# Kernel optimization log

Measured on AMD Instinct MI355X. Metric: run time of the kernel, lower is better.

## Reference

```python
import jax, jax.numpy as jnp
import numpy as np

LAMBDA_VIOLATION = 0.5
NUM_SAMPLES = 128
EPS = 1e-09
B = 4096
K_MAX = 128
NK_MAX = 128
# unique (n, k, m) parameter combos, cycled over the batch
COMBOS = np.array([[256, 128, 3], [192, 96, 3], [224, 112, 4], [160, 80, 2]], dtype=np.int64)


def setup_inputs() -> dict:
    key = jax.random.key(0)
    k1, k2, k3 = jax.random.split(key, 3)
    y_pred = jax.random.uniform(k1, (B, 1), minval=0.5, maxval=8.0, dtype=jnp.float32)
    y_true = jax.random.uniform(k2, (B, 1), minval=0.5, maxval=8.0, dtype=jnp.float32)
    P_padded = jax.random.normal(k3, (B, K_MAX, NK_MAX), dtype=jnp.float32)
    params = jnp.asarray(COMBOS[np.arange(B) % len(COMBOS)])  # [B, 3] int64
    return {"y_pred": y_pred, "y_true": y_true, "P_padded": P_padded, "params": params}


def reference(y_pred, y_true, P_padded, params):
    # LogMSE in base 2
    log2_pred = jnp.log2(jnp.clip(y_pred, EPS))
    log2_true = jnp.log2(jnp.clip(y_true, EPS))
    loss_logmse = jnp.mean((log2_true - log2_pred) ** 2)

    batch = P_padded.shape[0]
    p_np = np.asarray(params)  # int params are concrete constants
    combos, inverse = np.unique(p_np, axis=0, return_inverse=True)

    total_penalty = jnp.asarray(0.0, dtype=y_pred.dtype)
    xkey = jax.random.key(42)
    for i in range(combos.shape[0]):
        n, k, m = int(combos[i, 0]), int(combos[i, 1]), int(combos[i, 2])
        idx = np.nonzero(inverse == i)[0]
        if m + 1 > n or k <= 0 or n - k < 0 or idx.size == 0:
            continue
        g = idx.size
        P_actual = P_padded[idx, :k, : n - k]            # [g, k, n-k]
        X = jax.random.normal(jax.random.fold_in(xkey, i), (g, NUM_SAMPLES, k), dtype=y_pred.dtype)
        # G = [I_k | P_actual]  =>  C = X @ G = [X | X @ P_actual]
        C = jnp.concatenate([X, jnp.einsum('bsk,bkp->bsp', X, P_actual)], axis=2)  # [g, S, n]
        mags = jnp.abs(C)
        top, _ = jax.lax.top_k(mags, m + 1)              # [g, S, m+1] sorted descending
        hm = top[..., 0] / (top[..., m] + EPS)           # c_max / c_m
        max_hm = jnp.max(hm, axis=1)                     # [g]
        penalty = jax.nn.relu(max_hm - y_pred[idx].squeeze(-1))
        total_penalty = total_penalty + jnp.sum(penalty)

    loss_violation = total_penalty / batch
    total_loss = loss_logmse + LAMBDA_VIOLATION * loss_violation
    return total_loss, loss_logmse, loss_violation
```

## Files before the change

kernel.cpp:

```cpp
#include <hip/hip_runtime.h>
#include <stdint.h>

typedef short bf16x8 __attribute__((ext_vector_type(8)));
typedef float f32x4 __attribute__((ext_vector_type(4)));

__host__ __device__ inline uint32_t rotl32(uint32_t v, int d) {
  return (v << d) | (v >> (32 - d));
}

__host__ __device__ inline void tf2x32(uint32_t k0, uint32_t k1,
                                       uint32_t x0, uint32_t x1,
                                       uint32_t& o0, uint32_t& o1) {
  uint32_t ks0 = k0, ks1 = k1, ks2 = k0 ^ k1 ^ 0x1BD11BDAu;
  x0 += ks0; x1 += ks1;
#define TF_R(r) { x0 += x1; x1 = rotl32(x1, (r)); x1 ^= x0; }
  TF_R(13) TF_R(15) TF_R(26) TF_R(6)
  x0 += ks1; x1 += ks2 + 1u;
  TF_R(17) TF_R(29) TF_R(16) TF_R(24)
  x0 += ks2; x1 += ks0 + 2u;
  TF_R(13) TF_R(15) TF_R(26) TF_R(6)
  x0 += ks0; x1 += ks1 + 3u;
  TF_R(17) TF_R(29) TF_R(16) TF_R(24)
  x0 += ks1; x1 += ks2 + 4u;
  TF_R(13) TF_R(15) TF_R(26) TF_R(6)
  x0 += ks2; x1 += ks0 + 5u;
#undef TF_R
  o0 = x0; o1 = x1;
}

__device__ __forceinline__ float erfinv_xla(float x) {
  float w = -__logf(fmaf(-x, x, 1.0f));
  float p;
  if (w < 5.0f) {
    w = w - 2.5f;
    p = 2.81022636e-08f;
    p = fmaf(p, w, 3.43273939e-07f);
    p = fmaf(p, w, -3.5233877e-06f);
    p = fmaf(p, w, -4.39150654e-06f);
    p = fmaf(p, w, 0.00021858087f);
    p = fmaf(p, w, -0.00125372503f);
    p = fmaf(p, w, -0.00417768164f);
    p = fmaf(p, w, 0.246640727f);
    p = fmaf(p, w, 1.50140941f);
  } else {
    w = sqrtf(w) - 3.0f;
    p = -0.000200214257f;
    p = fmaf(p, w, 0.000100950558f);
    p = fmaf(p, w, 0.00134934322f);
    p = fmaf(p, w, -0.00367342844f);
    p = fmaf(p, w, 0.00573950773f);
    p = fmaf(p, w, -0.0076224613f);
    p = fmaf(p, w, 0.00943887047f);
    p = fmaf(p, w, 1.00167406f);
    p = fmaf(p, w, 2.83297682f);
  }
  return p * x;
}

__device__ __forceinline__ float bits_to_normal(uint32_t bits) {
  uint32_t fb = (bits >> 9) | 0x3F800000u;
  float f = __uint_as_float(fb) - 1.0f;
  const float lo = -0.99999994f;
  float u = fmaf(f, 1.0f - lo, lo);
  u = fmaxf(lo, u);
  return 1.41421356f * erfinv_xla(u);
}

__device__ __forceinline__ uint32_t cvt_pk_bf16(float lo, float hi) {
  uint32_t r;
  asm("v_cvt_pk_bf16_f32 %0, %1, %2" : "=v"(r) : "v"(lo), "v"(hi));
  return r;
}

__device__ __forceinline__ float bf2f_s(short h) {
  return __uint_as_float(((uint32_t)(uint16_t)h) << 16);
}

__device__ __forceinline__ bf16x8 pack8(const float (&r)[8]) {
  union { bf16x8 v; uint32_t u[4]; } o;
#pragma unroll
  for (int p = 0; p < 4; ++p)
    o.u[p] = cvt_pk_bf16(r[2 * p], r[2 * p + 1]);
  return o.v;
}

template <int T>
__device__ __forceinline__ void insT(float (&t)[T], float v) {
  if constexpr (T == 1) {
    t[0] = fmaxf(t[0], v);
  } else {
    float t0o = t[0], t1o = t[1];
    t[0] = fmaxf(t0o, v);
    t[1] = __builtin_amdgcn_fmed3f(v, t0o, t1o);
    float a = fminf(fminf(v, t0o), t1o);
#pragma unroll
    for (int q = 2; q < T; ++q) {
      float tq = t[q];
      t[q] = fmaxf(tq, a);
      a = fminf(tq, a);
    }
  }
}

template <int K, int KP, int T>
__device__ void process_combo(const float* __restrict__ Pp,
                              const float* __restrict__ yp,
                              const float* __restrict__ yt,
                              float* __restrict__ accum,
                              int ofs, uint32_t key0, uint32_t key1,
                              int rp, char* sm) {
  constexpr int KSTEPS = KP / 32;
  constexpr int NCH = (K + 31) / 32;
  constexpr int PH = K / 2;
  constexpr int ITERS = PH / 4;
  constexpr int XSTR = KP + 8;
  constexpr int XSTRU = XSTR / 2;
  constexpr int XROW_U = 64 * XSTRU;
  constexpr int REGION = 2 * 64 * XSTR * 2;
  constexpr bool SKIP1 = (K % 32) == 16;
  constexpr uint32_t HALF = 65536u * (uint32_t)K;

  const int tid = threadIdx.x;
  const int wave = tid >> 6;
  const int lane = tid & 63;
  const int quad = lane >> 4;
  const int l15 = lane & 15;
  const int row = wave >> 1;
  const int msub = (wave & 1) * 32;

  const int b0 = 4 * rp + ofs;
  const int b1 = 4 * (rp + 512) + ofs;

  uint32_t* Xu = (uint32_t*)sm;
  float* wvmax = (float*)(sm + REGION);
  float* maxhm = wvmax + 4;

  if (tid < 2) maxhm[tid] = 0.0f;

  const float* Pr = Pp + (size_t)(row ? b1 : b0) * 16384 + quad * (8 * 128) + l15;

  for (int pass = 0; pass < 2; ++pass) {
#pragma unroll
    for (int it = 0; it < ITERS; ++it) {
      int q = it * 256 + tid;
      int s_loc = q / PH;
      int k = 2 * (q - s_loc * PH);
      uint32_t ctr = (uint32_t)((rp * 128 + pass * 64 + s_loc) * K + k);
      uint32_t o0a, o1a, o0b, o1b;
      tf2x32(key0, key1, ctr, ctr + HALF, o0a, o1a);
      tf2x32(key0, key1, ctr + 1u, ctr + 1u + HALF, o0b, o1b);
      uint32_t idx = (uint32_t)(s_loc * XSTRU + (k >> 1));
      Xu[idx]          = cvt_pk_bf16(bits_to_normal(o0a), bits_to_normal(o0b));
      Xu[XROW_U + idx] = cvt_pk_bf16(bits_to_normal(o1a), bits_to_normal(o1b));
    }
    if constexpr (KP > K) {
      constexpr int PADU = (KP - K) / 2;
      for (int p = tid; p < 2 * 64 * PADU; p += 256) {
        int rs = p / PADU;
        int r = p - rs * PADU;
        Xu[rs * XSTRU + K / 2 + r] = 0;
      }
    }
    __syncthreads();

    bf16x8 ahi[2][KSTEPS];
#pragma unroll
    for (int f = 0; f < 2; ++f)
#pragma unroll
      for (int ks = 0; ks < KSTEPS; ++ks) {
        int off = ((row * 64 + msub + f * 16 + l15) * XSTR + ks * 32 + quad * 8) * 2;
        ahi[f][ks] = *(const bf16x8*)(sm + off);
      }
    float t5x[2][T];
#pragma unroll
    for (int f = 0; f < 2; ++f) {
#pragma unroll
      for (int q = 0; q < T; ++q) t5x[f][q] = 0.0f;
#pragma unroll
      for (int ks = 0; ks < KSTEPS; ++ks)
#pragma unroll
        for (int j = 0; j < 8; ++j)
          insT(t5x[f], fabsf(bf2f_s(ahi[f][ks][j])));
    }

    float t5y[2][T];
#pragma unroll
    for (int f = 0; f < 2; ++f)
#pragma unroll
      for (int q = 0; q < T; ++q) t5y[f][q] = 0.0f;

#pragma unroll 1
    for (int c = 0; c < NCH; ++c) {
      const bool skip1 = SKIP1 && (c == NCH - 1);
      const float* bpc = Pr + c * 32;
      f32x4 acc[2][2];
#pragma unroll
      for (int f = 0; f < 2; ++f)
#pragma unroll
        for (int nf = 0; nf < 2; ++nf) acc[f][nf] = (f32x4){0.f, 0.f, 0.f, 0.f};

#pragma unroll
      for (int ks = 0; ks < KSTEPS; ++ks) {
        const float* bpk = bpc + ks * (32 * 128);
        {
          float r0[8];
#pragma unroll
          for (int j = 0; j < 8; ++j) r0[j] = bpk[j * 128];
          bf16x8 bh0 = pack8(r0);
#pragma unroll
          for (int f = 0; f < 2; ++f)
            acc[f][0] = __builtin_amdgcn_mfma_f32_16x16x32_bf16(bh0, ahi[f][ks], acc[f][0], 0, 0, 0);
        }
        if (!skip1) {
          float r1[8];
#pragma unroll
          for (int j = 0; j < 8; ++j) r1[j] = bpk[j * 128 + 16];
          bf16x8 bh1 = pack8(r1);
#pragma unroll
          for (int f = 0; f < 2; ++f)
            acc[f][1] = __builtin_amdgcn_mfma_f32_16x16x32_bf16(bh1, ahi[f][ks], acc[f][1], 0, 0, 0);
        }
      }
#pragma unroll
      for (int f = 0; f < 2; ++f)
#pragma unroll
        for (int r = 0; r < 4; ++r) {
          insT(t5y[f], fabsf(acc[f][0][r]));
          if (!skip1) insT(t5y[f], fabsf(acc[f][1][r]));
        }
    }

    float wmax = 0.0f;
#pragma unroll
    for (int f = 0; f < 2; ++f) {
#pragma unroll
      for (int q = 0; q < T; ++q) insT(t5y[f], t5x[f][q]);
#pragma unroll
      for (int msk = 16; msk <= 32; msk <<= 1) {
        float o[T];
#pragma unroll
        for (int q = 0; q < T; ++q) o[q] = __shfl_xor(t5y[f][q], msk);
#pragma unroll
        for (int q = 0; q < T; ++q) insT(t5y[f], o[q]);
      }
      float hm = t5y[f][0] / (t5y[f][T - 1] + 1e-9f);
      wmax = fmaxf(wmax, hm);
    }
#pragma unroll
    for (int msk = 1; msk <= 8; msk <<= 1)
      wmax = fmaxf(wmax, __shfl_xor(wmax, msk));
    if (lane == 0) wvmax[wave] = wmax;
    __syncthreads();
    if (tid < 2)
      maxhm[tid] = fmaxf(maxhm[tid], fmaxf(wvmax[2 * tid], wvmax[2 * tid + 1]));
  }

  if (tid == 0) {
    float pen = fmaxf(maxhm[0] - yp[b0], 0.0f) + fmaxf(maxhm[1] - yp[b1], 0.0f);
    atomicAdd(&accum[0], pen);
    float d0 = log2f(fmaxf(yt[b0], 1e-9f)) - log2f(fmaxf(yp[b0], 1e-9f));
    float d1 = log2f(fmaxf(yt[b1], 1e-9f)) - log2f(fmaxf(yp[b1], 1e-9f));
    atomicAdd(&accum[1], fmaf(d0, d0, d1 * d1));
  }
}

struct ComboArgs {
  int ofs[4];
  uint32_t k0[4];
  uint32_t k1[4];
};

#define SM_BYTES (34816 + 16 + 8)

__global__ __launch_bounds__(256, 2)
void viol_kernel(const float* __restrict__ Pp, const float* __restrict__ yp,
                 const float* __restrict__ yt, float* __restrict__ accum,
                 ComboArgs ca) {
  __shared__ __align__(16) char sm[SM_BYTES];
  int i = blockIdx.x >> 9;
  int rp = blockIdx.x & 511;
  switch (i) {
    case 0: process_combo< 80,  96, 3>(Pp, yp, yt, accum, ca.ofs[0], ca.k0[0], ca.k1[0], rp, sm); break;
    case 1: process_combo< 96,  96, 4>(Pp, yp, yt, accum, ca.ofs[1], ca.k0[1], ca.k1[1], rp, sm); break;
    case 2: process_combo<112, 128, 5>(Pp, yp, yt, accum, ca.ofs[2], ca.k0[2], ca.k1[2], rp, sm); break;
    default: process_combo<128, 128, 4>(Pp, yp, yt, accum, ca.ofs[3], ca.k0[3], ca.k1[3], rp, sm); break;
  }
}

__global__ void finalize_kernel(const float* __restrict__ accum, float* __restrict__ out) {
  if (threadIdx.x == 0 && blockIdx.x == 0) {
    float viol = accum[0] / 4096.0f;
    float lm = accum[1] / 4096.0f;
    out[0] = fmaf(0.5f, viol, lm);
    out[1] = lm;
    out[2] = viol;
  }
}

extern "C" void kernel_launch(void* const* d_in, const int* in_sizes, int n_in,
                              void* d_out, int out_size, void* d_ws, size_t ws_size,
                              hipStream_t stream) {
  const float* y_pred   = (const float*)d_in[0];
  const float* y_true   = (const float*)d_in[1];
  const float* P_padded = (const float*)d_in[2];
  float* accum = (float*)d_ws;
  float* out = (float*)d_out;

  hipMemsetAsync(accum, 0, 2 * sizeof(float), stream);

  ComboArgs ca;
  const int ofs[4] = {3, 1, 2, 0};
  for (int i = 0; i < 4; ++i) {
    ca.ofs[i] = ofs[i];
    uint32_t o0, o1;
    tf2x32(0u, 42u, 0u, (uint32_t)i, o0, o1);
    ca.k0[i] = o0;
    ca.k1[i] = o1;
  }

  viol_kernel<<<2048, 256, 0, stream>>>(P_padded, y_pred, y_true, accum, ca);
  finalize_kernel<<<1, 64, 0, stream>>>(accum, out);
}
```

Measured before the change: 461.8 us.

## Software-pipeline P tile loads across MFMA steps with rotating register buffers

Replaces the per-step load-then-MFMA pattern in the chunk loop with a rotating set of 3-4 register buffers. Each step issues the global load for the tile DD steps ahead, prefetching into the next chunk, and starts the first loads before X generation. This hides global load latency behind MFMAs and the Threefry RNG work. The skip1 path no longer skips loads and MFMAs for the padded half-tile, so it does extra work and reads beyond the valid columns. That adds register pressure and may change the top-k over the padded columns.

```diff
diff --git a/kernel.cpp b/kernel.cpp
--- a/kernel.cpp
+++ b/kernel.cpp
@@ -119,6 +119,8 @@
   constexpr int REGION = 2 * 64 * XSTR * 2;
   constexpr bool SKIP1 = (K % 32) == 16;
   constexpr uint32_t HALF = 65536u * (uint32_t)K;
+  constexpr int TPC = 2 * KSTEPS;
+  constexpr int DD = (TPC % 4 == 0) ? 4 : 3;
 
   const int tid = threadIdx.x;
   const int wave = tid >> 6;
@@ -140,6 +142,18 @@
   const float* Pr = Pp + (size_t)(row ? b1 : b0) * 16384 + quad * (8 * 128) + l15;
 
   for (int pass = 0; pass < 2; ++pass) {
+    float buf0[8], buf1[8], buf2[8], buf3[8];
+#pragma unroll
+    for (int j = 0; j < 8; ++j) buf0[j] = Pr[j * 128];
+#pragma unroll
+    for (int j = 0; j < 8; ++j) buf1[j] = Pr[16 + j * 128];
+#pragma unroll
+    for (int j = 0; j < 8; ++j) buf2[j] = Pr[4096 + j * 128];
+    if constexpr (DD == 4) {
+#pragma unroll
+      for (int j = 0; j < 8; ++j) buf3[j] = Pr[4096 + 16 + j * 128];
+    }
+
 #pragma unroll
     for (int it = 0; it < ITERS; ++it) {
       int q = it * 256 + tid;
@@ -191,36 +205,35 @@
 
 #pragma unroll 1
     for (int c = 0; c < NCH; ++c) {
+      const float* bpc = Pr + c * 32;
+      const float* bpn = Pr + (c + 1 < NCH ? c + 1 : c) * 32;
+      f32x4 acc[2][2];
+#pragma unroll
+      for (int f = 0; f < 2; ++f)
+#pragma unroll
+        for (int nf = 0; nf < 2; ++nf) acc[f][nf] = (f32x4){0.f, 0.f, 0.f, 0.f};
+
+      auto step = [&](int p, float (&buf)[8]) {
+        const int ks = p >> 1, nf = p & 1;
+        bf16x8 bh = pack8(buf);
+        const int p2 = p + DD;
+        const float* na = (p2 < TPC)
+            ? (bpc + (p2 >> 1) * 4096 + (p2 & 1) * 16)
+            : (bpn + ((p2 - TPC) >> 1) * 4096 + ((p2 - TPC) & 1) * 16);
+#pragma unroll
+        for (int j = 0; j < 8; ++j) buf[j] = na[j * 128];
+        acc[0][nf] = __builtin_amdgcn_mfma_f32_16x16x32_bf16(bh, ahi[0][ks], acc[0][nf], 0, 0, 0);
+        acc[1][nf] = __builtin_amdgcn_mfma_f32_16x16x32_bf16(bh, ahi[1][ks], acc[1][nf], 0, 0, 0);
+      };
+#pragma unroll
+      for (int pb = 0; pb < TPC; pb += DD) {
+        step(pb + 0, buf0);
+        step(pb + 1, buf1);
+        step(pb + 2, buf2);
+        if constexpr (DD == 4) step(pb + 3, buf3);
+      }
+
       const bool skip1 = SKIP1 && (c == NCH - 1);
-      const float* bpc = Pr + c * 32;
-      f32x4 acc[2][2];
-#pragma unroll
-      for (int f = 0; f < 2; ++f)
-#pragma unroll
-        for (int nf = 0; nf < 2; ++nf) acc[f][nf] = (f32x4){0.f, 0.f, 0.f, 0.f};
-
-#pragma unroll
-      for (int ks = 0; ks < KSTEPS; ++ks) {
-        const float* bpk = bpc + ks * (32 * 128);
-        {
-          float r0[8];
-#pragma unroll
-          for (int j = 0; j < 8; ++j) r0[j] = bpk[j * 128];
-          bf16x8 bh0 = pack8(r0);
-#pragma unroll
-          for (int f = 0; f < 2; ++f)
-            acc[f][0] = __builtin_amdgcn_mfma_f32_16x16x32_bf16(bh0, ahi[f][ks], acc[f][0], 0, 0, 0);
-        }
-        if (!skip1) {
-          float r1[8];
-#pragma unroll
-          for (int j = 0; j < 8; ++j) r1[j] = bpk[j * 128 + 16];
-          bf16x8 bh1 = pack8(r1);
-#pragma unroll
-          for (int f = 0; f < 2; ++f)
-            acc[f][1] = __builtin_amdgcn_mfma_f32_16x16x32_bf16(bh1, ahi[f][ks], acc[f][1], 0, 0, 0);
-        }
-      }
 #pragma unroll
       for (int f = 0; f < 2; ++f)
 #pragma unroll
```

Measured after the change: 728.1 us. 57.7% more time.
